# Kernel optimization log

Hardware: AMD Instinct MI355X
Metric: run time of the kernel (lower is better)

Reference implementation:

```python
import jax, jax.numpy as jnp
import numpy as np

HIDDEN = 64
HALF = 32
VOCAB = 64
B, L = 256, 2048


def _l2norm(x):
    # matches torch F.normalize(dim=-1, eps=1e-12)
    return x / jnp.maximum(jnp.linalg.norm(x, axis=-1, keepdims=True), 1e-12)


def setup_inputs() -> dict:
    key = jax.random.key(0)
    ks = jax.random.split(key, 16)
    s = 0.02
    return {
        "seq": jax.random.randint(ks[0], (B, L), 0, VOCAB),
        "embed": jax.random.normal(ks[1], (VOCAB, HIDDEN), jnp.float32) * s,
        "W1": jax.random.normal(ks[2], (2 * HIDDEN, HIDDEN), jnp.float32) * s,
        "b1": jnp.zeros((2 * HIDDEN,), jnp.float32),
        "W2": jax.random.normal(ks[3], (HIDDEN, 2 * HIDDEN), jnp.float32) * s,
        "b2": jnp.zeros((HIDDEN,), jnp.float32),
        "ln_g": jnp.ones((HIDDEN,), jnp.float32),
        "ln_b": jnp.zeros((HIDDEN,), jnp.float32),
        "Ws": jax.random.normal(ks[4], (HALF, HIDDEN), jnp.float32) * s,
        "bs": jnp.zeros((HALF,), jnp.float32),
        "We": jax.random.normal(ks[5], (HALF, HIDDEN), jnp.float32) * s,
        "be": jnp.zeros((HALF,), jnp.float32),
        "Wrp": jax.random.normal(ks[6], (HIDDEN, 2 * HALF), jnp.float32) * s,
        "brp": jnp.zeros((HIDDEN,), jnp.float32),
        "Wo": jax.random.normal(ks[7], (VOCAB, HIDDEN), jnp.float32) * s,
        "bo": jnp.zeros((VOCAB,), jnp.float32),
    }


def reference(seq, embed, W1, b1, W2, b2, ln_g, ln_b, Ws, bs, We, be, Wrp, brp, Wo, bo):
    # Encoder: embed -> LayerNorm(h + FF(h))
    h0 = embed[seq]                                     # [B,L,H]
    ff = jnp.maximum(h0 @ W1.T + b1, 0.0) @ W2.T + b2
    x = h0 + ff
    mu = x.mean(-1, keepdims=True)
    var = x.var(-1, keepdims=True)
    h = (x - mu) / jnp.sqrt(var + 1e-5) * ln_g + ln_b   # [B,L,H]

    Bn, Ln, _ = h.shape
    half = Ws.shape[0]
    hs_all = h @ Ws.T + bs                              # [B,L,half]
    he_all = h @ We.T + be

    # sequential delta-rule memory writes over t = 0 .. L-2
    hs_seq = jnp.swapaxes(hs_all[:, :-1], 0, 1)         # [L-1,B,half]
    he_seq = jnp.swapaxes(he_all[:, :-1], 0, 1)
    scales = (jnp.arange(1, Ln) / Ln).astype(h.dtype)   # (t+1)/L
    M0 = jnp.zeros((Bn, half, half), h.dtype)

    def step(carry, inp):
        M_s, M_e = carry
        hs, he, sc = inp
        ks_ = _l2norm(hs)
        ke_ = _l2norm(he)
        vps = jnp.einsum('bij,bj->bi', M_s, ks_)
        vpe = jnp.einsum('bij,bj->bi', M_e, ke_)
        M_s = M_s + (hs - vps)[:, :, None] * ks_[:, None, :]
        M_e = M_e + sc * (he - vpe)[:, :, None] * ke_[:, None, :]
        return (M_s, M_e), None

    (M_s, M_e), _ = jax.lax.scan(step, (M0, M0), (hs_seq, he_seq, scales))

    # read with last-position query
    qs = _l2norm(hs_all[:, -1])
    qe = _l2norm(he_all[:, -1])
    rs = jnp.einsum('bij,bj->bi', M_s, qs)
    re = jnp.einsum('bij,bj->bi', M_e, qe)
    r = jnp.concatenate([rs, re], axis=-1)              # [B, 2*half]
    return (r @ Wrp.T + brp) @ Wo.T + bo                # [B, vocab]
```

## Files before the change

kernel.cpp:

```cpp
#include <hip/hip_runtime.h>

#define HIDDEN 64
#define HALFD  32
#define VOCAB  64
#define BATCH  256
#define SEQLEN 2048

#define RLF(v, sl) __int_as_float(__builtin_amdgcn_readlane(__float_as_int(v), (sl)))
#define RLI(v, sl) __builtin_amdgcn_readlane((v), (sl))

__global__ __launch_bounds__(64) void vocab_kernel(
    const float* __restrict__ embed, const float* __restrict__ W1, const float* __restrict__ b1,
    const float* __restrict__ W2, const float* __restrict__ b2,
    const float* __restrict__ ln_g, const float* __restrict__ ln_b,
    const float* __restrict__ Ws, const float* __restrict__ bs,
    const float* __restrict__ We, const float* __restrict__ be,
    float* __restrict__ ws)
{
    const int v = blockIdx.x;
    const int tid = threadIdx.x;

    __shared__ float e_s[64];
    __shared__ float a1_s[128];
    __shared__ float h_s[64];

    e_s[tid] = embed[v * 64 + tid];
    __syncthreads();

    float acc0 = b1[tid], acc1 = b1[tid + 64];
    #pragma unroll 8
    for (int m = 0; m < 64; ++m) {
        float ev = e_s[m];
        acc0 = fmaf(ev, W1[tid * 64 + m], acc0);
        acc1 = fmaf(ev, W1[(tid + 64) * 64 + m], acc1);
    }
    a1_s[tid]      = fmaxf(acc0, 0.0f);
    a1_s[tid + 64] = fmaxf(acc1, 0.0f);
    __syncthreads();

    float ff = b2[tid];
    #pragma unroll 8
    for (int m = 0; m < 128; ++m) ff = fmaf(a1_s[m], W2[tid * 128 + m], ff);
    float x = e_s[tid] + ff;

    float s = x, s2 = x * x;
    #pragma unroll
    for (int off = 32; off >= 1; off >>= 1) {
        s  += __shfl_xor(s,  off, 64);
        s2 += __shfl_xor(s2, off, 64);
    }
    float mu  = s * (1.0f / 64.0f);
    float var = s2 * (1.0f / 64.0f) - mu * mu;
    float hval = (x - mu) * rsqrtf(var + 1e-5f) * ln_g[tid] + ln_b[tid];
    h_s[tid] = hval;
    __syncthreads();

    const int j = tid & 31;
    const bool is_s = tid < 32;
    const float* W = is_s ? Ws : We;
    float acc = is_s ? bs[j] : be[j];
    #pragma unroll 8
    for (int m = 0; m < 64; ++m) acc = fmaf(h_s[m], W[j * 64 + m], acc);

    float n2 = acc * acc;
    #pragma unroll
    for (int off = 16; off >= 1; off >>= 1) n2 += __shfl_xor(n2, off, 64);
    float norm = sqrtf(n2);
    float kn = acc / fmaxf(norm, 1e-12f);

    const int base = v * 32 + j;
    if (is_s) { ws[base]        = kn; ws[4096 + base] = acc; }
    else      { ws[2048 + base] = kn; ws[6144 + base] = acc; }
}

__global__ __launch_bounds__(256) void gram_kernel(float* __restrict__ ws)
{
    const int w = blockIdx.x;
    const int tid = threadIdx.x;
    __shared__ float k_s[2048];
    const float* kb = ws + w * 2048;
    for (int i = tid; i < 2048; i += 256) k_s[i] = kb[i];
    __syncthreads();
    const int a  = tid >> 2;
    const int b0 = (tid & 3) << 4;
    float* Gw = ws + 8192 + w * 4096 + a * 64;
    for (int bb = 0; bb < 16; ++bb) {
        const int bcol = b0 + bb;
        float acc = 0.f;
        #pragma unroll
        for (int m = 0; m < 32; ++m) acc = fmaf(k_s[a * 32 + m], k_s[bcol * 32 + m], acc);
        Gw[bcol] = acc;
    }
}

__global__ __launch_bounds__(128) void scan_kernel(
    const int* __restrict__ seq, const float* __restrict__ ws,
    const float* __restrict__ Wrp, const float* __restrict__ brp,
    const float* __restrict__ Wo, const float* __restrict__ bo,
    float* __restrict__ out)
{
    const int b    = blockIdx.x;
    const int tid  = threadIdx.x;
    const int w    = tid >> 6;
    const int lane = tid & 63;
    const int l7   = lane & 7;
    const bool is_e = (w == 1);

    __shared__ float wacc_s[2][64];
    __shared__ float r_s[64];
    __shared__ float t1_s[64];

    const int*   sq = seq + b * SEQLEN;
    const float* Gg = ws + 8192 + w * 4096;

    const float invL = 1.0f / (float)SEQLEN;

    int tokvC = sq[2040 + l7];
    int tk0 = RLI(tokvC, 0), tk1 = RLI(tokvC, 1), tk2 = RLI(tokvC, 2), tk3 = RLI(tokvC, 3);
    int tk4 = RLI(tokvC, 4), tk5 = RLI(tokvC, 5), tk6 = RLI(tokvC, 6), tk7 = RLI(tokvC, 7);

    float grow0 = Gg[tk0 * 64 + lane], grow1 = Gg[tk1 * 64 + lane];
    float grow2 = Gg[tk2 * 64 + lane], grow3 = Gg[tk3 * 64 + lane];
    float grow4 = Gg[tk4 * 64 + lane], grow5 = Gg[tk5 * 64 + lane];
    float grow6 = Gg[tk6 * 64 + lane], grow7 = Gg[tk7 * 64 + lane];

    int tokvN = sq[2032 + l7];

    float u = Gg[tk7 * 64 + lane];
    float waccv = 0.0f;

    for (int c = 255; c >= 0; --c) {
        float bp = __shfl(u, tokvC, 64);

        int nk0 = RLI(tokvN, 0), nk1 = RLI(tokvN, 1), nk2 = RLI(tokvN, 2), nk3 = RLI(tokvN, 3);
        int nk4 = RLI(tokvN, 4), nk5 = RLI(tokvN, 5), nk6 = RLI(tokvN, 6), nk7 = RLI(tokvN, 7);
        float gn0 = Gg[nk0 * 64 + lane], gn1 = Gg[nk1 * 64 + lane];
        float gn2 = Gg[nk2 * 64 + lane], gn3 = Gg[nk3 * 64 + lane];
        float gn4 = Gg[nk4 * 64 + lane], gn5 = Gg[nk5 * 64 + lane];
        float gn6 = Gg[nk6 * 64 + lane], gn7 = Gg[nk7 * 64 + lane];
        int cm2 = (c >= 2) ? (c - 2) : 0;
        int tokv2 = sq[cm2 * 8 + l7];

        float g01 = RLF(grow0, tk1), g02 = RLF(grow0, tk2), g03 = RLF(grow0, tk3);
        float g04 = RLF(grow0, tk4), g05 = RLF(grow0, tk5), g06 = RLF(grow0, tk6), g07 = RLF(grow0, tk7);
        float g12 = RLF(grow1, tk2), g13 = RLF(grow1, tk3), g14 = RLF(grow1, tk4);
        float g15 = RLF(grow1, tk5), g16 = RLF(grow1, tk6), g17 = RLF(grow1, tk7);
        float g23 = RLF(grow2, tk3), g24 = RLF(grow2, tk4), g25 = RLF(grow2, tk5);
        float g26 = RLF(grow2, tk6), g27 = RLF(grow2, tk7);
        float g34 = RLF(grow3, tk4), g35 = RLF(grow3, tk5), g36 = RLF(grow3, tk6), g37 = RLF(grow3, tk7);
        float g45 = RLF(grow4, tk5), g46 = RLF(grow4, tk6), g47 = RLF(grow4, tk7);
        float g56 = RLF(grow5, tk6), g57 = RLF(grow5, tk7);
        float g67 = RLF(grow6, tk7);

        float t0 = RLF(bp, 0), t1 = RLF(bp, 1), t2 = RLF(bp, 2), t3 = RLF(bp, 3);
        float t4 = RLF(bp, 4), t5 = RLF(bp, 5), t6 = RLF(bp, 6), t7 = RLF(bp, 7);

        float fb = (float)(8 * c + 1) * invL;
        float f0 = is_e ? fb            : 1.0f;
        float f1 = is_e ? fb +     invL : 1.0f;
        float f2 = is_e ? fb + 2 * invL : 1.0f;
        float f3 = is_e ? fb + 3 * invL : 1.0f;
        float f4 = is_e ? fb + 4 * invL : 1.0f;
        float f5 = is_e ? fb + 5 * invL : 1.0f;
        float f6 = is_e ? fb + 6 * invL : 1.0f;
        float f7 = (c == 255) ? 0.0f : (is_e ? fb + 7 * invL : 1.0f);

        float s7 = f7 * t7;
        float s6 = f6 * (t6 - g67 * s7);
        float s5 = f5 * ((t5 - g57 * s7) - g56 * s6);
        float s4 = f4 * (((t4 - g47 * s7) - g46 * s6) - g45 * s5);
        float s3 = f3 * ((((t3 - g37 * s7) - g36 * s6) - g35 * s5) - g34 * s4);
        float s2 = f2 * (((((t2 - g27 * s7) - g26 * s6) - g25 * s5) - g24 * s4) - g23 * s3);
        float s1 = f1 * ((((((t1 - g17 * s7) - g16 * s6) - g15 * s5) - g14 * s4) - g13 * s3) - g12 * s2);
        float s0 = f0 * (((((((t0 - g07 * s7) - g06 * s6) - g05 * s5) - g04 * s4) - g03 * s3) - g02 * s2) - g01 * s1);

        {
            float A = fmaf(grow0, s0, fmaf(grow1, s1, fmaf(grow2, s2, grow3 * s3)));
            float B = fmaf(grow4, s4, fmaf(grow5, s5, fmaf(grow6, s6, grow7 * s7)));
            u -= (A + B);
        }

        waccv += (lane == tk0) ? s0 : 0.0f;
        waccv += (lane == tk1) ? s1 : 0.0f;
        waccv += (lane == tk2) ? s2 : 0.0f;
        waccv += (lane == tk3) ? s3 : 0.0f;
        waccv += (lane == tk4) ? s4 : 0.0f;
        waccv += (lane == tk5) ? s5 : 0.0f;
        waccv += (lane == tk6) ? s6 : 0.0f;
        waccv += (lane == tk7) ? s7 : 0.0f;

        tk0 = nk0; tk1 = nk1; tk2 = nk2; tk3 = nk3;
        tk4 = nk4; tk5 = nk5; tk6 = nk6; tk7 = nk7;
        grow0 = gn0; grow1 = gn1; grow2 = gn2; grow3 = gn3;
        grow4 = gn4; grow5 = gn5; grow6 = gn6; grow7 = gn7;
        tokvC = tokvN; tokvN = tokv2;
    }

    wacc_s[w][lane] = waccv;
    __syncthreads();

    if (tid < 64) {
        const int w2  = tid >> 5;
        const int rho = tid & 31;
        const float* vv = ws + 4096 + w2 * 2048;
        const float* wa = &wacc_s[w2][0];
        float acc = 0.0f;
        #pragma unroll 8
        for (int tok = 0; tok < 64; ++tok) acc = fmaf(wa[tok], vv[tok * 32 + rho], acc);
        r_s[tid] = acc;
    }
    __syncthreads();

    if (tid < 64) {
        float acc = brp[tid];
        #pragma unroll 8
        for (int m = 0; m < 64; ++m) acc = fmaf(Wrp[tid * 64 + m], r_s[m], acc);
        t1_s[tid] = acc;
    }
    __syncthreads();
    if (tid < 64) {
        float acc = bo[tid];
        #pragma unroll 8
        for (int m = 0; m < 64; ++m) acc = fmaf(Wo[tid * 64 + m], t1_s[m], acc);
        out[b * 64 + tid] = acc;
    }
}

extern "C" void kernel_launch(void* const* d_in, const int* in_sizes, int n_in,
                              void* d_out, int out_size, void* d_ws, size_t ws_size,
                              hipStream_t stream)
{
    const int*   seq   = (const int*)  d_in[0];
    const float* embed = (const float*)d_in[1];
    const float* W1    = (const float*)d_in[2];
    const float* b1    = (const float*)d_in[3];
    const float* W2    = (const float*)d_in[4];
    const float* b2    = (const float*)d_in[5];
    const float* ln_g  = (const float*)d_in[6];
    const float* ln_b  = (const float*)d_in[7];
    const float* Ws    = (const float*)d_in[8];
    const float* bs    = (const float*)d_in[9];
    const float* We    = (const float*)d_in[10];
    const float* be    = (const float*)d_in[11];
    const float* Wrp   = (const float*)d_in[12];
    const float* brp   = (const float*)d_in[13];
    const float* Wo    = (const float*)d_in[14];
    const float* bo    = (const float*)d_in[15];
    float* ws  = (float*)d_ws;
    float* out = (float*)d_out;

    hipLaunchKernelGGL(vocab_kernel, dim3(VOCAB), dim3(64), 0, stream,
                       embed, W1, b1, W2, b2, ln_g, ln_b, Ws, bs, We, be, ws);
    hipLaunchKernelGGL(gram_kernel, dim3(2), dim3(256), 0, stream, ws);
    hipLaunchKernelGGL(scan_kernel, dim3(BATCH), dim3(128), 0, stream,
                       seq, ws, Wrp, brp, Wo, bo, out);
}
```

Measured before the change: 233.2 us.

## Precompute per-chunk triangular inverse matrices in LDS to shorten the serial scan

Before the scan, each lane builds for its chunks the 8x8 upper-triangular matrix that maps the projected values to the chunk update coefficients, folding in the Gram entries and the scale factors. These matrices go into shared memory along with the token sequence. The serial loop then replaces the dependent back-substitution chain and its 28 readlanes with a shallow matrix-vector product. Loads are double-buffered through two Chunk structs with the loop unrolled by two. This adds a parallel precompute phase, about 82KB of LDS and more registers per thread, in exchange for a shorter dependency chain per step.

Result: faster. 211.1 us (-9.5%).

```diff
diff --git a/kernel.cpp b/kernel.cpp
--- a/kernel.cpp
+++ b/kernel.cpp
@@ -8,6 +8,8 @@
 
 #define RLF(v, sl) __int_as_float(__builtin_amdgcn_readlane(__float_as_int(v), (sl)))
 #define RLI(v, sl) __builtin_amdgcn_readlane((v), (sl))
+#define GIX(j,m) (((j)==0?0:(j)==1?7:(j)==2?13:(j)==3?18:(j)==4?22:(j)==5?25:27) + (m) - (j) - 1)
+#define OM(m) (((m)*((m)+1))>>1)
 
 __global__ __launch_bounds__(64) void vocab_kernel(
     const float* __restrict__ embed, const float* __restrict__ W1, const float* __restrict__ b1,
@@ -92,6 +94,13 @@
         Gw[bcol] = acc;
     }
 }
+
+struct Chunk {
+    int   tokv;
+    int   tk[8];
+    float grow[8];
+    float W[36];
+};
 
 __global__ __launch_bounds__(128) void scan_kernel(
     const int* __restrict__ seq, const float* __restrict__ ws,
@@ -106,94 +115,142 @@
     const int l7   = lane & 7;
     const bool is_e = (w == 1);
 
+    __shared__ __align__(16) float Wtab[2 * 256 * 36];
+    __shared__ __align__(16) int   toklds[SEQLEN];
     __shared__ float wacc_s[2][64];
     __shared__ float r_s[64];
     __shared__ float t1_s[64];
 
-    const int*   sq = seq + b * SEQLEN;
-    const float* Gg = ws + 8192 + w * 4096;
-
-    const float invL = 1.0f / (float)SEQLEN;
-
-    int tokvC = sq[2040 + l7];
-    int tk0 = RLI(tokvC, 0), tk1 = RLI(tokvC, 1), tk2 = RLI(tokvC, 2), tk3 = RLI(tokvC, 3);
-    int tk4 = RLI(tokvC, 4), tk5 = RLI(tokvC, 5), tk6 = RLI(tokvC, 6), tk7 = RLI(tokvC, 7);
-
-    float grow0 = Gg[tk0 * 64 + lane], grow1 = Gg[tk1 * 64 + lane];
-    float grow2 = Gg[tk2 * 64 + lane], grow3 = Gg[tk3 * 64 + lane];
-    float grow4 = Gg[tk4 * 64 + lane], grow5 = Gg[tk5 * 64 + lane];
-    float grow6 = Gg[tk6 * 64 + lane], grow7 = Gg[tk7 * 64 + lane];
-
-    int tokvN = sq[2032 + l7];
-
-    float u = Gg[tk7 * 64 + lane];
-    float waccv = 0.0f;
-
-    for (int c = 255; c >= 0; --c) {
-        float bp = __shfl(u, tokvC, 64);
-
-        int nk0 = RLI(tokvN, 0), nk1 = RLI(tokvN, 1), nk2 = RLI(tokvN, 2), nk3 = RLI(tokvN, 3);
-        int nk4 = RLI(tokvN, 4), nk5 = RLI(tokvN, 5), nk6 = RLI(tokvN, 6), nk7 = RLI(tokvN, 7);
-        float gn0 = Gg[nk0 * 64 + lane], gn1 = Gg[nk1 * 64 + lane];
-        float gn2 = Gg[nk2 * 64 + lane], gn3 = Gg[nk3 * 64 + lane];
-        float gn4 = Gg[nk4 * 64 + lane], gn5 = Gg[nk5 * 64 + lane];
-        float gn6 = Gg[nk6 * 64 + lane], gn7 = Gg[nk7 * 64 + lane];
-        int cm2 = (c >= 2) ? (c - 2) : 0;
-        int tokv2 = sq[cm2 * 8 + l7];
-
-        float g01 = RLF(grow0, tk1), g02 = RLF(grow0, tk2), g03 = RLF(grow0, tk3);
-        float g04 = RLF(grow0, tk4), g05 = RLF(grow0, tk5), g06 = RLF(grow0, tk6), g07 = RLF(grow0, tk7);
-        float g12 = RLF(grow1, tk2), g13 = RLF(grow1, tk3), g14 = RLF(grow1, tk4);
-        float g15 = RLF(grow1, tk5), g16 = RLF(grow1, tk6), g17 = RLF(grow1, tk7);
-        float g23 = RLF(grow2, tk3), g24 = RLF(grow2, tk4), g25 = RLF(grow2, tk5);
-        float g26 = RLF(grow2, tk6), g27 = RLF(grow2, tk7);
-        float g34 = RLF(grow3, tk4), g35 = RLF(grow3, tk5), g36 = RLF(grow3, tk6), g37 = RLF(grow3, tk7);
-        float g45 = RLF(grow4, tk5), g46 = RLF(grow4, tk6), g47 = RLF(grow4, tk7);
-        float g56 = RLF(grow5, tk6), g57 = RLF(grow5, tk7);
-        float g67 = RLF(grow6, tk7);
+    const float* Gg     = ws + 8192 + w * 4096;
+    float*       Wtab_w = Wtab + w * (256 * 36);
+
+    {
+        const int4* sq4 = (const int4*)(seq + b * SEQLEN);
+        int4* tl = (int4*)toklds;
+        #pragma unroll
+        for (int i = 0; i < 4; ++i) tl[tid + i * 128] = sq4[tid + i * 128];
+    }
+    __syncthreads();
+
+    {
+        const float invL = 1.0f / (float)SEQLEN;
+        #pragma unroll
+        for (int qq = 0; qq < 4; ++qq) {
+            const int c = lane + (qq << 6);
+            int tj[8];
+            #pragma unroll
+            for (int j = 0; j < 8; ++j) tj[j] = toklds[c * 8 + j];
+
+            float f[8];
+            float fb = (float)(8 * c + 1) * invL;
+            #pragma unroll
+            for (int j = 0; j < 8; ++j) f[j] = is_e ? (fb + (float)j * invL) : 1.0f;
+            if (c == 255) f[7] = 0.0f;
+
+            float g[28];
+            #pragma unroll
+            for (int j = 0; j < 7; ++j)
+                #pragma unroll
+                for (int m = j + 1; m < 8; ++m) g[GIX(j, m)] = Gg[tj[j] * 64 + tj[m]];
+
+            float Wp[36];
+            #pragma unroll
+            for (int m = 0; m < 8; ++m) {
+                float col[8];
+                col[m] = f[m];
+                #pragma unroll
+                for (int j = 6; j >= 0; --j) {
+                    if (j < m) {
+                        float acc = 0.0f;
+                        #pragma unroll
+                        for (int p = 1; p < 8; ++p)
+                            if (p > j && p <= m) acc = fmaf(g[GIX(j, p)], col[p], acc);
+                        col[j] = -f[j] * acc;
+                    }
+                }
+                #pragma unroll
+                for (int j = 0; j < 8; ++j)
+                    if (j <= m) Wp[OM(m) + j] = col[j];
+            }
+
+            float4* dst = (float4*)&Wtab_w[c * 36];
+            #pragma unroll
+            for (int i = 0; i < 9; ++i)
+                dst[i] = make_float4(Wp[4*i], Wp[4*i+1], Wp[4*i+2], Wp[4*i+3]);
+        }
+    }
+    __syncthreads();
+
+    Chunk A, B;
+    float u, waccv = 0.0f;
+
+    A.tokv = toklds[2040 + l7];
+    #pragma unroll
+    for (int j = 0; j < 8; ++j) A.tk[j] = RLI(A.tokv, j);
+    #pragma unroll
+    for (int j = 0; j < 8; ++j) A.grow[j] = Gg[A.tk[j] * 64 + lane];
+    {
+        const float4* wsrc = (const float4*)&Wtab_w[255 * 36];
+        #pragma unroll
+        for (int i = 0; i < 9; ++i) {
+            float4 v = wsrc[i];
+            A.W[4*i] = v.x; A.W[4*i+1] = v.y; A.W[4*i+2] = v.z; A.W[4*i+3] = v.w;
+        }
+    }
+    B.tokv = toklds[2032 + l7];
+    u = Gg[A.tk[7] * 64 + lane];
+
+    auto body = [&](Chunk& cur, Chunk& nxt, int c) {
+        float bp = __shfl(u, cur.tokv, 64);
+
+        const int cm1 = (c > 0) ? c - 1 : 0;
+        const int cm2 = (c > 1) ? c - 2 : 0;
+        #pragma unroll
+        for (int j = 0; j < 8; ++j) nxt.tk[j] = RLI(nxt.tokv, j);
+        #pragma unroll
+        for (int j = 0; j < 8; ++j) nxt.grow[j] = Gg[nxt.tk[j] * 64 + lane];
+        {
+            const float4* wsrc = (const float4*)&Wtab_w[cm1 * 36];
+            #pragma unroll
+            for (int i = 0; i < 9; ++i) {
+                float4 v = wsrc[i];
+                nxt.W[4*i] = v.x; nxt.W[4*i+1] = v.y; nxt.W[4*i+2] = v.z; nxt.W[4*i+3] = v.w;
+            }
+        }
+        int tokv2 = toklds[cm2 * 8 + l7];
 
         float t0 = RLF(bp, 0), t1 = RLF(bp, 1), t2 = RLF(bp, 2), t3 = RLF(bp, 3);
         float t4 = RLF(bp, 4), t5 = RLF(bp, 5), t6 = RLF(bp, 6), t7 = RLF(bp, 7);
 
-        float fb = (float)(8 * c + 1) * invL;
-        float f0 = is_e ? fb            : 1.0f;
-        float f1 = is_e ? fb +     invL : 1.0f;
-        float f2 = is_e ? fb + 2 * invL : 1.0f;
-        float f3 = is_e ? fb + 3 * invL : 1.0f;
-        float f4 = is_e ? fb + 4 * invL : 1.0f;
-        float f5 = is_e ? fb + 5 * invL : 1.0f;
-        float f6 = is_e ? fb + 6 * invL : 1.0f;
-        float f7 = (c == 255) ? 0.0f : (is_e ? fb + 7 * invL : 1.0f);
-
-        float s7 = f7 * t7;
-        float s6 = f6 * (t6 - g67 * s7);
-        float s5 = f5 * ((t5 - g57 * s7) - g56 * s6);
-        float s4 = f4 * (((t4 - g47 * s7) - g46 * s6) - g45 * s5);
-        float s3 = f3 * ((((t3 - g37 * s7) - g36 * s6) - g35 * s5) - g34 * s4);
-        float s2 = f2 * (((((t2 - g27 * s7) - g26 * s6) - g25 * s5) - g24 * s4) - g23 * s3);
-        float s1 = f1 * ((((((t1 - g17 * s7) - g16 * s6) - g15 * s5) - g14 * s4) - g13 * s3) - g12 * s2);
-        float s0 = f0 * (((((((t0 - g07 * s7) - g06 * s6) - g05 * s5) - g04 * s4) - g03 * s3) - g02 * s2) - g01 * s1);
-
-        {
-            float A = fmaf(grow0, s0, fmaf(grow1, s1, fmaf(grow2, s2, grow3 * s3)));
-            float B = fmaf(grow4, s4, fmaf(grow5, s5, fmaf(grow6, s6, grow7 * s7)));
-            u -= (A + B);
-        }
-
-        waccv += (lane == tk0) ? s0 : 0.0f;
-        waccv += (lane == tk1) ? s1 : 0.0f;
-        waccv += (lane == tk2) ? s2 : 0.0f;
-        waccv += (lane == tk3) ? s3 : 0.0f;
-        waccv += (lane == tk4) ? s4 : 0.0f;
-        waccv += (lane == tk5) ? s5 : 0.0f;
-        waccv += (lane == tk6) ? s6 : 0.0f;
-        waccv += (lane == tk7) ? s7 : 0.0f;
-
-        tk0 = nk0; tk1 = nk1; tk2 = nk2; tk3 = nk3;
-        tk4 = nk4; tk5 = nk5; tk6 = nk6; tk7 = nk7;
-        grow0 = gn0; grow1 = gn1; grow2 = gn2; grow3 = gn3;
-        grow4 = gn4; grow5 = gn5; grow6 = gn6; grow7 = gn7;
-        tokvC = tokvN; tokvN = tokv2;
+        const float* W = cur.W;
+        float s7 = W[35] * t7;
+        float s6 = fmaf(W[27], t6, W[34] * t7);
+        float s5 = fmaf(W[20], t5, W[26] * t6) + W[33] * t7;
+        float s4 = fmaf(W[14], t4, W[19] * t5) + fmaf(W[25], t6, W[32] * t7);
+        float s3 = fmaf(W[9],  t3, W[13] * t4) + fmaf(W[18], t5, fmaf(W[24], t6, W[31] * t7));
+        float s2 = fmaf(W[5],  t2, W[8]  * t3) + fmaf(W[12], t4, W[17] * t5) + fmaf(W[23], t6, W[30] * t7);
+        float s1 = fmaf(W[2],  t1, W[4]  * t2) + fmaf(W[7],  t3, W[11] * t4) + fmaf(W[16], t5, fmaf(W[22], t6, W[29] * t7));
+        float s0 = fmaf(W[0],  t0, W[1]  * t1) + fmaf(W[3],  t2, W[6]  * t3) + fmaf(W[10], t4, W[15] * t5) + fmaf(W[21], t6, W[28] * t7);
+
+        float dA = fmaf(cur.grow[0], s0, fmaf(cur.grow[1], s1, fmaf(cur.grow[2], s2, cur.grow[3] * s3)));
+        float dB = fmaf(cur.grow[4], s4, fmaf(cur.grow[5], s5, fmaf(cur.grow[6], s6, cur.grow[7] * s7)));
+        u -= (dA + dB);
+
+        waccv += (lane == cur.tk[0]) ? s0 : 0.0f;
+        waccv += (lane == cur.tk[1]) ? s1 : 0.0f;
+        waccv += (lane == cur.tk[2]) ? s2 : 0.0f;
+        waccv += (lane == cur.tk[3]) ? s3 : 0.0f;
+        waccv += (lane == cur.tk[4]) ? s4 : 0.0f;
+        waccv += (lane == cur.tk[5]) ? s5 : 0.0f;
+        waccv += (lane == cur.tk[6]) ? s6 : 0.0f;
+        waccv += (lane == cur.tk[7]) ? s7 : 0.0f;
+
+        cur.tokv = tokv2;
+    };
+
+    for (int c = 255; c >= 1; c -= 2) {
+        body(A, B, c);
+        body(B, A, c - 1);
     }
 
     wacc_s[w][lane] = waccv;
```

## Double-buffer Gram row prefetch and load tokens as scalars in scan loop

Applied to the files above, without the earlier changes.

Restructures the scan loop into a two-step unrolled body that ping-pongs between two Gram-row register buffers, prefetching rows two chunks ahead instead of one. Token ids are now loaded as uniform scalar loads rather than via readlane from a vector load, and the bp shuffle for the next chunk is issued right after u is updated. The aim is to hide global-load latency on the serial dependency chain, at the cost of more registers, with launch bounds set to one block per CU minimum.

Measured after the change: 255.5 us. 9.6% more time.

```diff
diff --git a/kernel.cpp b/kernel.cpp
--- a/kernel.cpp
+++ b/kernel.cpp
@@ -7,7 +7,6 @@
 #define SEQLEN 2048
 
 #define RLF(v, sl) __int_as_float(__builtin_amdgcn_readlane(__float_as_int(v), (sl)))
-#define RLI(v, sl) __builtin_amdgcn_readlane((v), (sl))
 
 __global__ __launch_bounds__(64) void vocab_kernel(
     const float* __restrict__ embed, const float* __restrict__ W1, const float* __restrict__ b1,
@@ -93,7 +92,7 @@
     }
 }
 
-__global__ __launch_bounds__(128) void scan_kernel(
+__global__ __launch_bounds__(128, 1) void scan_kernel(
     const int* __restrict__ seq, const float* __restrict__ ws,
     const float* __restrict__ Wrp, const float* __restrict__ brp,
     const float* __restrict__ Wo, const float* __restrict__ bo,
@@ -110,50 +109,48 @@
     __shared__ float r_s[64];
     __shared__ float t1_s[64];
 
+    const float* Gg = ws + 8192 + w * 4096;
     const int*   sq = seq + b * SEQLEN;
-    const float* Gg = ws + 8192 + w * 4096;
 
     const float invL = 1.0f / (float)SEQLEN;
 
+    int tkC[8], tkN[8], tkI[8];
+    float grA[8], grB[8];
+
+    #pragma unroll
+    for (int j = 0; j < 8; ++j) tkC[j] = sq[2040 + j];
+    #pragma unroll
+    for (int j = 0; j < 8; ++j) tkN[j] = sq[2032 + j];
+    #pragma unroll
+    for (int j = 0; j < 8; ++j) grA[j] = Gg[tkC[j] * 64 + lane];
+    #pragma unroll
+    for (int j = 0; j < 8; ++j) grB[j] = Gg[tkN[j] * 64 + lane];
     int tokvC = sq[2040 + l7];
-    int tk0 = RLI(tokvC, 0), tk1 = RLI(tokvC, 1), tk2 = RLI(tokvC, 2), tk3 = RLI(tokvC, 3);
-    int tk4 = RLI(tokvC, 4), tk5 = RLI(tokvC, 5), tk6 = RLI(tokvC, 6), tk7 = RLI(tokvC, 7);
-
-    float grow0 = Gg[tk0 * 64 + lane], grow1 = Gg[tk1 * 64 + lane];
-    float grow2 = Gg[tk2 * 64 + lane], grow3 = Gg[tk3 * 64 + lane];
-    float grow4 = Gg[tk4 * 64 + lane], grow5 = Gg[tk5 * 64 + lane];
-    float grow6 = Gg[tk6 * 64 + lane], grow7 = Gg[tk7 * 64 + lane];
-
     int tokvN = sq[2032 + l7];
 
-    float u = Gg[tk7 * 64 + lane];
+    float u = Gg[tkC[7] * 64 + lane];
+    float braw = __shfl(u, tokvC, 64);
     float waccv = 0.0f;
 
-    for (int c = 255; c >= 0; --c) {
-        float bp = __shfl(u, tokvC, 64);
-
-        int nk0 = RLI(tokvN, 0), nk1 = RLI(tokvN, 1), nk2 = RLI(tokvN, 2), nk3 = RLI(tokvN, 3);
-        int nk4 = RLI(tokvN, 4), nk5 = RLI(tokvN, 5), nk6 = RLI(tokvN, 6), nk7 = RLI(tokvN, 7);
-        float gn0 = Gg[nk0 * 64 + lane], gn1 = Gg[nk1 * 64 + lane];
-        float gn2 = Gg[nk2 * 64 + lane], gn3 = Gg[nk3 * 64 + lane];
-        float gn4 = Gg[nk4 * 64 + lane], gn5 = Gg[nk5 * 64 + lane];
-        float gn6 = Gg[nk6 * 64 + lane], gn7 = Gg[nk7 * 64 + lane];
-        int cm2 = (c >= 2) ? (c - 2) : 0;
-        int tokv2 = sq[cm2 * 8 + l7];
-
-        float g01 = RLF(grow0, tk1), g02 = RLF(grow0, tk2), g03 = RLF(grow0, tk3);
-        float g04 = RLF(grow0, tk4), g05 = RLF(grow0, tk5), g06 = RLF(grow0, tk6), g07 = RLF(grow0, tk7);
-        float g12 = RLF(grow1, tk2), g13 = RLF(grow1, tk3), g14 = RLF(grow1, tk4);
-        float g15 = RLF(grow1, tk5), g16 = RLF(grow1, tk6), g17 = RLF(grow1, tk7);
-        float g23 = RLF(grow2, tk3), g24 = RLF(grow2, tk4), g25 = RLF(grow2, tk5);
-        float g26 = RLF(grow2, tk6), g27 = RLF(grow2, tk7);
-        float g34 = RLF(grow3, tk4), g35 = RLF(grow3, tk5), g36 = RLF(grow3, tk6), g37 = RLF(grow3, tk7);
-        float g45 = RLF(grow4, tk5), g46 = RLF(grow4, tk6), g47 = RLF(grow4, tk7);
-        float g56 = RLF(grow5, tk6), g57 = RLF(grow5, tk7);
-        float g67 = RLF(grow6, tk7);
-
-        float t0 = RLF(bp, 0), t1 = RLF(bp, 1), t2 = RLF(bp, 2), t3 = RLF(bp, 3);
-        float t4 = RLF(bp, 4), t5 = RLF(bp, 5), t6 = RLF(bp, 6), t7 = RLF(bp, 7);
+    auto body = [&](int c, float (&gr)[8]) {
+        const int cm2 = (c >= 2) ? (c - 2) : 0;
+        #pragma unroll
+        for (int j = 0; j < 8; ++j) tkI[j] = sq[cm2 * 8 + j];
+        int tokvI = sq[cm2 * 8 + l7];
+
+        float t0 = RLF(braw, 0), t1 = RLF(braw, 1), t2 = RLF(braw, 2), t3 = RLF(braw, 3);
+        float t4 = RLF(braw, 4), t5 = RLF(braw, 5), t6 = RLF(braw, 6), t7 = RLF(braw, 7);
+
+        float g01 = RLF(gr[0], tkC[1]), g02 = RLF(gr[0], tkC[2]), g03 = RLF(gr[0], tkC[3]);
+        float g04 = RLF(gr[0], tkC[4]), g05 = RLF(gr[0], tkC[5]), g06 = RLF(gr[0], tkC[6]), g07 = RLF(gr[0], tkC[7]);
+        float g12 = RLF(gr[1], tkC[2]), g13 = RLF(gr[1], tkC[3]), g14 = RLF(gr[1], tkC[4]);
+        float g15 = RLF(gr[1], tkC[5]), g16 = RLF(gr[1], tkC[6]), g17 = RLF(gr[1], tkC[7]);
+        float g23 = RLF(gr[2], tkC[3]), g24 = RLF(gr[2], tkC[4]), g25 = RLF(gr[2], tkC[5]);
+        float g26 = RLF(gr[2], tkC[6]), g27 = RLF(gr[2], tkC[7]);
+        float g34 = RLF(gr[3], tkC[4]), g35 = RLF(gr[3], tkC[5]), g36 = RLF(gr[3], tkC[6]), g37 = RLF(gr[3], tkC[7]);
+        float g45 = RLF(gr[4], tkC[5]), g46 = RLF(gr[4], tkC[6]), g47 = RLF(gr[4], tkC[7]);
+        float g56 = RLF(gr[5], tkC[6]), g57 = RLF(gr[5], tkC[7]);
+        float g67 = RLF(gr[6], tkC[7]);
 
         float fb = (float)(8 * c + 1) * invL;
         float f0 = is_e ? fb            : 1.0f;
@@ -174,26 +171,32 @@
         float s1 = f1 * ((((((t1 - g17 * s7) - g16 * s6) - g15 * s5) - g14 * s4) - g13 * s3) - g12 * s2);
         float s0 = f0 * (((((((t0 - g07 * s7) - g06 * s6) - g05 * s5) - g04 * s4) - g03 * s3) - g02 * s2) - g01 * s1);
 
-        {
-            float A = fmaf(grow0, s0, fmaf(grow1, s1, fmaf(grow2, s2, grow3 * s3)));
-            float B = fmaf(grow4, s4, fmaf(grow5, s5, fmaf(grow6, s6, grow7 * s7)));
-            u -= (A + B);
-        }
-
-        waccv += (lane == tk0) ? s0 : 0.0f;
-        waccv += (lane == tk1) ? s1 : 0.0f;
-        waccv += (lane == tk2) ? s2 : 0.0f;
-        waccv += (lane == tk3) ? s3 : 0.0f;
-        waccv += (lane == tk4) ? s4 : 0.0f;
-        waccv += (lane == tk5) ? s5 : 0.0f;
-        waccv += (lane == tk6) ? s6 : 0.0f;
-        waccv += (lane == tk7) ? s7 : 0.0f;
-
-        tk0 = nk0; tk1 = nk1; tk2 = nk2; tk3 = nk3;
-        tk4 = nk4; tk5 = nk5; tk6 = nk6; tk7 = nk7;
-        grow0 = gn0; grow1 = gn1; grow2 = gn2; grow3 = gn3;
-        grow4 = gn4; grow5 = gn5; grow6 = gn6; grow7 = gn7;
-        tokvC = tokvN; tokvN = tokv2;
+        float dA = fmaf(gr[0], s0, fmaf(gr[1], s1, fmaf(gr[2], s2, gr[3] * s3)));
+        float dB = fmaf(gr[4], s4, fmaf(gr[5], s5, fmaf(gr[6], s6, gr[7] * s7)));
+        u -= (dA + dB);
+
+        braw = __shfl(u, tokvN, 64);
+
+        waccv += (lane == tkC[0]) ? s0 : 0.0f;
+        waccv += (lane == tkC[1]) ? s1 : 0.0f;
+        waccv += (lane == tkC[2]) ? s2 : 0.0f;
+        waccv += (lane == tkC[3]) ? s3 : 0.0f;
+        waccv += (lane == tkC[4]) ? s4 : 0.0f;
+        waccv += (lane == tkC[5]) ? s5 : 0.0f;
+        waccv += (lane == tkC[6]) ? s6 : 0.0f;
+        waccv += (lane == tkC[7]) ? s7 : 0.0f;
+
+        #pragma unroll
+        for (int j = 0; j < 8; ++j) gr[j] = Gg[tkI[j] * 64 + lane];
+
+        #pragma unroll
+        for (int j = 0; j < 8; ++j) { tkC[j] = tkN[j]; tkN[j] = tkI[j]; }
+        tokvN = tokvI;
+    };
+
+    for (int c = 255; c >= 1; c -= 2) {
+        body(c, grA);
+        body(c - 1, grB);
     }
 
     wacc_s[w][lane] = waccv;
```
